# Kernel optimization log

Measured on AMD Instinct MI355X. Metric: run time of the kernel, lower is better.

The kernel has to match this reference:

```python
import jax, jax.numpy as jnp
import numpy as np
from jax import lax

B, C, H0, W0 = 8, 128, 62, 62
G, K, DIL, STRIDE, PAD = 4, 3, 1, 1, 1
P = K * K
GC = C // G
OFFSET_SCALE = 1.0


def setup_inputs() -> dict:
    key = jax.random.key(0)
    ks = jax.random.split(key, 10)
    s = 0.05
    return {
        "x": jax.random.normal(ks[0], (B, C, H0, W0), jnp.float32),
        "conv_w": jax.random.normal(ks[1], (C, C, 1, 1), jnp.float32) * s,
        "conv_b": jax.random.normal(ks[2], (C,), jnp.float32) * s,
        "in_proj_w": jax.random.normal(ks[3], (C, C), jnp.float32) * s,
        "in_proj_b": jnp.zeros((C,), jnp.float32),
        "dw_w": jax.random.normal(ks[4], (C, 1, K, K), jnp.float32) * s,
        "dw_b": jnp.zeros((C,), jnp.float32),
        "ln_g": jnp.ones((C,), jnp.float32),
        "ln_b": jnp.zeros((C,), jnp.float32),
        "off_w": jax.random.normal(ks[5], (C, G * P * 2), jnp.float32) * s,
        "off_b": jax.random.normal(ks[6], (G * P * 2,), jnp.float32) * s,
        "mask_w": jax.random.normal(ks[7], (C, G * P), jnp.float32) * s,
        "mask_b": jnp.zeros((G * P,), jnp.float32),
        "out_proj_w": jax.random.normal(ks[8], (C, C), jnp.float32) * s,
        "out_proj_b": jnp.zeros((C,), jnp.float32),
    }


def _bilinear_sample(img, ix, iy, Hp, Wp):
    # img: [B, G, Hp*Wp, GC] flattened spatial; ix, iy: [B, G, Q, P] pixel coords.
    # Matches torch grid_sample(bilinear, zeros, align_corners=False).
    x0 = jnp.floor(ix)
    y0 = jnp.floor(iy)

    def gather(xi, yi):
        valid = (xi >= 0) & (xi <= Wp - 1) & (yi >= 0) & (yi <= Hp - 1)
        xc = jnp.clip(xi, 0, Wp - 1).astype(jnp.int32)
        yc = jnp.clip(yi, 0, Hp - 1).astype(jnp.int32)
        lin = (yc * Wp + xc).reshape(img.shape[0], img.shape[1], -1)  # [B,G,Q*P]
        v = jnp.take_along_axis(img, lin[..., None], axis=2)          # [B,G,Q*P,GC]
        v = v.reshape(xi.shape + (img.shape[-1],))
        return v * valid[..., None].astype(img.dtype)

    wx1 = (ix - x0)[..., None]
    wx0 = 1.0 - wx1
    wy1 = (iy - y0)[..., None]
    wy0 = 1.0 - wy1
    return (gather(x0, y0) * wx0 * wy0
            + gather(x0 + 1.0, y0) * wx1 * wy0
            + gather(x0, y0 + 1.0) * wx0 * wy1
            + gather(x0 + 1.0, y0 + 1.0) * wx1 * wy1)


def _dcnv3_core(x_proj, offset, mask):
    # x_proj: [B,H,W,C] NHWC; offset: [B,H,W,G*P*2]; mask: [B,H,W,G*P] (softmaxed)
    Bn, H, W, _ = x_proj.shape
    xp = jnp.pad(x_proj, ((0, 0), (PAD, PAD), (PAD, PAD), (0, 0)))
    Hp, Wp = H + 2 * PAD, W + 2 * PAD  # H_out == H for K=3, PAD=1, STRIDE=1
    # reference points (normalized to padded size)
    ref_x = (jnp.arange(W, dtype=jnp.float32) * STRIDE + (DIL * (K - 1)) / 2.0 + 0.5) / Wp
    ref_y = (jnp.arange(H, dtype=jnp.float32) * STRIDE + (DIL * (K - 1)) / 2.0 + 0.5) / Hp
    ref = jnp.stack(jnp.broadcast_arrays(ref_x[None, :], ref_y[:, None]), -1)  # [H,W,2] (x,y)
    # dilation grid (same ordering as torch.meshgrid(x_lin, y_lin))
    klin = (jnp.arange(K, dtype=jnp.float32) * DIL - (DIL * (K - 1)) // 2)
    gx, gy = jnp.meshgrid(klin, klin, indexing='ij')
    grid = jnp.stack([gx / Wp, gy / Hp], -1).reshape(P, 2)
    grid = jnp.tile(grid[None], (G, 1, 1)).reshape(G * P, 2)
    spatial_norm = jnp.array([Wp, Hp], jnp.float32)
    loc = (ref[:, :, None, :] + grid[None, None] * OFFSET_SCALE)[None] \
        + offset.reshape(Bn, H, W, G * P, 2) * OFFSET_SCALE / spatial_norm
    g = 2.0 * loc - 1.0  # normalized grid in [-1,1]
    ix = ((g[..., 0] + 1.0) * Wp - 1.0) / 2.0  # align_corners=False unnormalize
    iy = ((g[..., 1] + 1.0) * Hp - 1.0) / 2.0
    Q = H * W
    ix = ix.reshape(Bn, Q, G, P).transpose(0, 2, 1, 3)  # [B,G,Q,P]
    iy = iy.reshape(Bn, Q, G, P).transpose(0, 2, 1, 3)
    img = xp.reshape(Bn, Hp * Wp, G, GC).transpose(0, 2, 1, 3)  # [B,G,S,GC]
    sampled = _bilinear_sample(img, ix, iy, Hp, Wp)             # [B,G,Q,P,GC]
    m = mask.reshape(Bn, Q, G, P).transpose(0, 2, 1, 3)
    out = jnp.einsum('bgqpc,bgqp->bqgc', sampled, m)
    return out.reshape(Bn, H, W, G * GC)


def reference(x, conv_w, conv_b, in_proj_w, in_proj_b, dw_w, dw_b, ln_g, ln_b,
              off_w, off_b, mask_w, mask_b, out_proj_w, out_proj_b):
    dn = ('NCHW', 'OIHW', 'NCHW')
    # 1x1 conv with padding=1 (spatial grows by 2 on each dim)
    y = lax.conv_general_dilated(x, conv_w, (1, 1), ((PAD, PAD), (PAD, PAD)),
                                 dimension_numbers=dn) + conv_b[None, :, None, None]
    t = y.transpose(0, 2, 3, 1)  # NHWC
    x_proj = t @ in_proj_w + in_proj_b
    # offset/mask branch: depthwise conv + LayerNorm + GELU
    d = lax.conv_general_dilated(y, dw_w, (1, 1), ((1, 1), (1, 1)),
                                 dimension_numbers=dn,
                                 feature_group_count=C) + dw_b[None, :, None, None]
    d = d.transpose(0, 2, 3, 1)
    mu = d.mean(-1, keepdims=True)
    var = ((d - mu) ** 2).mean(-1, keepdims=True)
    d = (d - mu) / jnp.sqrt(var + 1e-5) * ln_g + ln_b
    d = jax.nn.gelu(d, approximate=False)
    offset = d @ off_w + off_b
    Bn, H, W, _ = d.shape
    m = jax.nn.softmax((d @ mask_w + mask_b).reshape(Bn, H, W, G, P), axis=-1)
    out = _dcnv3_core(x_proj, offset, m.reshape(Bn, H, W, G * P))
    out = out @ out_proj_w + out_proj_b
    return out.transpose(0, 3, 1, 2)  # back to NCHW
```

## Files before the change

### kernel.cpp

```cpp
#include <hip/hip_runtime.h>
#include <math.h>

#define BB 8
#define CH 128
#define HH 64
#define WWID 64
#define HIN 62
#define WIN 62
#define SPIN (HIN*WIN)
#define HP 66
#define WP 66
#define GG 4
#define GCH 32
#define NPIX (BB*HH*WWID)
#define ASTRIDE 136

typedef _Float16 v8h __attribute__((ext_vector_type(8)));
typedef _Float16 v4h __attribute__((ext_vector_type(4)));
typedef float    v4f __attribute__((ext_vector_type(4)));

__global__ __launch_bounds__(256) void p0_pack(const float* __restrict__ conv_w,
                                               const float* __restrict__ in_proj_w,
                                               const float* __restrict__ off_w,
                                               const float* __restrict__ mask_w,
                                               const float* __restrict__ out_proj_w,
                                               const float* __restrict__ dw_w,
                                               _Float16* __restrict__ wp,
                                               float* __restrict__ dwT) {
    int t = threadIdx.x;
    if (blockIdx.x == 31) {
        if (t < 128) {
            #pragma unroll
            for (int tap = 0; tap < 9; tap++) dwT[tap * 128 + t] = dw_w[t * 9 + tap];
        }
        return;
    }
    int tid = blockIdx.x * 256 + t;
    int mat, base;
    if (tid < 2048)      { mat = 0; base = 0; }
    else if (tid < 4096) { mat = 1; base = 2048; }
    else if (tid < 5888) { mat = 2; base = 4096; }
    else                 { mat = 3; base = 5888; }
    int fi = tid - base;
    int nt = fi >> 8, rem = fi & 255, kc = rem >> 6, lane = rem & 63;
    int n = nt * 16 + (lane & 15);
    int kbase = kc * 32 + ((lane >> 4) & 3) * 8;
    _Float16* dst = wp + (size_t)tid * 8;
    #pragma unroll
    for (int j = 0; j < 8; j++) {
        int k = kbase + j;
        float v;
        if (mat == 0)      v = conv_w[n * CH + k];
        else if (mat == 1) v = in_proj_w[k * CH + n];
        else if (mat == 2) v = (n < 72) ? off_w[k * 72 + n]
                               : (n < 108 ? mask_w[k * 36 + (n - 72)] : 0.f);
        else               v = out_proj_w[k * CH + n];
        dst[j] = (_Float16)v;
    }
}

__device__ inline void mfma_loop8(const _Float16* __restrict__ a16,
                                  const _Float16* __restrict__ wp,
                                  v4f acc[4], int t) {
    int lane = t & 63;
    int wv = t >> 6;
    int mt = wv >> 1, ntb = (wv & 1) * 4;
    const _Float16* abase = a16 + (mt * 16 + (lane & 15)) * ASTRIDE + ((lane >> 4) * 8);
    #pragma unroll
    for (int kc = 0; kc < 4; kc++) {
        v8h av = *(const v8h*)(abase + kc * 32);
        #pragma unroll
        for (int j = 0; j < 4; j++) {
            v8h bv = *(const v8h*)(wp + ((size_t)((ntb + j) * 4 + kc) * 64 + lane) * 8);
            acc[j] = __builtin_amdgcn_mfma_f32_16x16x32_f16(av, bv, acc[j], 0, 0, 0);
        }
    }
}

__device__ inline void acc_to_a16_8(_Float16* a16, v4f acc[4], int t) {
    int lane = t & 63, ncol = lane & 15;
    int wv = t >> 6;
    int m0 = (wv >> 1) * 16 + ((lane >> 4) * 4);
    int ntb = (wv & 1) * 4;
    #pragma unroll
    for (int j = 0; j < 4; j++)
        #pragma unroll
        for (int r = 0; r < 4; r++)
            a16[(m0 + r) * ASTRIDE + (ntb + j) * 16 + ncol] = (_Float16)acc[j][r];
}

__global__ __launch_bounds__(512) void gA_conv_inproj(const float* __restrict__ x,
                                                      const _Float16* __restrict__ wp_conv,
                                                      const _Float16* __restrict__ wp_in,
                                                      const float* __restrict__ conv_b,
                                                      const float* __restrict__ in_b,
                                                      _Float16* __restrict__ y16,
                                                      _Float16* __restrict__ xpad16) {
    __shared__ _Float16 a16[64 * ASTRIDE];
    int pix0 = blockIdx.x * 64;
    int t = threadIdx.x;
    int h = (pix0 >> 6) & 63, b = pix0 >> 12;
    bool hin = (h >= 1 && h <= 62);
    for (int q = t; q < 8192; q += 512) {
        int c = q >> 6, w = q & 63;
        float v = 0.f;
        if (hin && w >= 1 && w <= 62)
            v = x[((size_t)(b * CH + c)) * SPIN + (h - 1) * WIN + (w - 1)];
        a16[w * ASTRIDE + c] = (_Float16)v;
    }
    __syncthreads();
    int lane = t & 63, ncol = lane & 15;
    int ntb = ((t >> 6) & 1) * 4;
    v4f acc[4];
    #pragma unroll
    for (int j = 0; j < 4; j++) {
        float bv = conv_b[(ntb + j) * 16 + ncol];
        acc[j] = (v4f){bv, bv, bv, bv};
    }
    mfma_loop8(a16, wp_conv, acc, t);
    __syncthreads();
    acc_to_a16_8(a16, acc, t);
    __syncthreads();
    {
        _Float16* dst = y16 + (size_t)pix0 * CH;
        for (int q = t; q < 1024; q += 512)
            *(v8h*)&dst[q * 8] = *(const v8h*)&a16[(q >> 4) * ASTRIDE + (q & 15) * 8];
    }
    v4f acc2[4];
    #pragma unroll
    for (int j = 0; j < 4; j++) {
        float bv = in_b[(ntb + j) * 16 + ncol];
        acc2[j] = (v4f){bv, bv, bv, bv};
    }
    mfma_loop8(a16, wp_in, acc2, t);
    __syncthreads();
    acc_to_a16_8(a16, acc2, t);
    __syncthreads();
    {
        _Float16* dst = xpad16 + (size_t)(((b * HP) + h + 1) * WP + 1) * CH;
        for (int q = t; q < 1024; q += 512)
            *(v8h*)&dst[q * 8] = *(const v8h*)&a16[(q >> 4) * ASTRIDE + (q & 15) * 8];
    }
}

__global__ __launch_bounds__(512) void gF_dwln_offmask(const _Float16* __restrict__ y16,
                                                       const _Float16* __restrict__ wp_om,
                                                       const float* __restrict__ dwT,
                                                       const float* __restrict__ dw_b,
                                                       const float* __restrict__ ln_g,
                                                       const float* __restrict__ ln_b,
                                                       const float* __restrict__ off_b,
                                                       const float* __restrict__ mask_b,
                                                       float* __restrict__ tapmeta) {
    __shared__ char smem[49920];
    _Float16* ylds = (_Float16*)smem;
    int t = threadIdx.x;
    int pix0 = blockIdx.x * 64;
    int h = (pix0 >> 6) & 63, b = pix0 >> 12;
    if (h == 0 || h == 63) {
        for (int i = t; i < 3120; i += 512) *(v8h*)&ylds[i * 8] = (v8h)(_Float16)0;
        __syncthreads();
    }
    for (int idx = t; idx < 3072; idx += 512) {
        int r = idx >> 10, w = (idx >> 4) & 63, c8 = idx & 15;
        int hh = h + r - 1;
        if (hh >= 0 && hh <= 63) {
            v8h v = *(const v8h*)&y16[(size_t)(((b * 64 + hh) * 64 + w) * CH) + c8 * 8];
            *(v8h*)&ylds[(size_t)((r * 16 + c8) * 65 + w) * 8] = v;
        }
    }
    __syncthreads();
    int px = t >> 3, q8 = t & 7;
    float acc[16];
    #pragma unroll
    for (int cb = 0; cb < 4; cb++) *(float4*)&acc[cb * 4] = *(const float4*)&dw_b[q8 * 16 + cb * 4];
    #pragma unroll
    for (int r = 0; r < 3; r++) {
        #pragma unroll
        for (int kx = 0; kx < 3; kx++) {
            int wq = px + kx - 1;
            bool valid = (wq >= 0 && wq <= 63);
            int wpc = min(max(wq, 0), 63);
            int tap = r * 3 + kx;
            if (valid) {
                #pragma unroll
                for (int cb = 0; cb < 2; cb++) {
                    v8h yv = *(const v8h*)&ylds[(size_t)((r * 16 + q8 * 2 + cb) * 65 + wpc) * 8];
                    float4 wa = *(const float4*)&dwT[tap * 128 + q8 * 16 + cb * 8];
                    float4 wb = *(const float4*)&dwT[tap * 128 + q8 * 16 + cb * 8 + 4];
                    acc[cb*8+0] += (float)yv[0] * wa.x; acc[cb*8+1] += (float)yv[1] * wa.y;
                    acc[cb*8+2] += (float)yv[2] * wa.z; acc[cb*8+3] += (float)yv[3] * wa.w;
                    acc[cb*8+4] += (float)yv[4] * wb.x; acc[cb*8+5] += (float)yv[5] * wb.y;
                    acc[cb*8+6] += (float)yv[6] * wb.z; acc[cb*8+7] += (float)yv[7] * wb.w;
                }
            }
        }
    }
    float s = 0.f, ss = 0.f;
    #pragma unroll
    for (int j = 0; j < 16; j++) { s += acc[j]; ss += acc[j] * acc[j]; }
    s  += __shfl_xor(s, 1);  s  += __shfl_xor(s, 2);  s  += __shfl_xor(s, 4);
    ss += __shfl_xor(ss, 1); ss += __shfl_xor(ss, 2); ss += __shfl_xor(ss, 4);
    float mu = s * (1.f / 128.f);
    float var = ss * (1.f / 128.f) - mu * mu;
    float rstd = rsqrtf(var + 1e-5f);
    v8h dreg[2];
    #pragma unroll
    for (int cb = 0; cb < 2; cb++) {
        float4 ga = *(const float4*)&ln_g[q8 * 16 + cb * 8];
        float4 gb = *(const float4*)&ln_g[q8 * 16 + cb * 8 + 4];
        float4 ba = *(const float4*)&ln_b[q8 * 16 + cb * 8];
        float4 bb = *(const float4*)&ln_b[q8 * 16 + cb * 8 + 4];
        float gv[8] = {ga.x, ga.y, ga.z, ga.w, gb.x, gb.y, gb.z, gb.w};
        float bv[8] = {ba.x, ba.y, ba.z, ba.w, bb.x, bb.y, bb.z, bb.w};
        #pragma unroll
        for (int j = 0; j < 8; j++) {
            float xln = (acc[cb * 8 + j] - mu) * rstd * gv[j] + bv[j];
            float gel = 0.5f * xln * (1.f + erff(xln * 0.70710678118654752f));
            dreg[cb][j] = (_Float16)gel;
        }
    }
    __syncthreads();
    _Float16* a16 = (_Float16*)smem;
    float* om = (float*)(smem + 17408);
    #pragma unroll
    for (int cb = 0; cb < 2; cb++)
        *(v8h*)&a16[px * ASTRIDE + q8 * 16 + cb * 8] = dreg[cb];
    __syncthreads();
    int lane = t & 63, ncol = lane & 15;
    int ntb = ((t >> 6) & 1) * 4;
    v4f macc[4];
    #pragma unroll
    for (int j = 0; j < 4; j++) {
        int n = (ntb + j) * 16 + ncol;
        float bv = (n < 72) ? off_b[n] : (n < 108 ? mask_b[n - 72] : 0.f);
        macc[j] = (v4f){bv, bv, bv, bv};
    }
    mfma_loop8(a16, wp_om, macc, t);
    int m0 = ((t >> 6) >> 1) * 16 + ((lane >> 4) * 4);
    #pragma unroll
    for (int j = 0; j < 4; j++) {
        if (ntb + j < 7) {
            #pragma unroll
            for (int r = 0; r < 4; r++)
                om[(m0 + r) * 112 + (ntb + j) * 16 + ncol] = macc[j][r];
        }
    }
    __syncthreads();
    if (t < 256) {
        int pxs = t >> 2, gx = t & 3;
        const float* row = &om[pxs * 112];
        float lg[9];
        #pragma unroll
        for (int i = 0; i < 9; i++) lg[i] = row[72 + gx * 9 + i];
        float mx = lg[0];
        #pragma unroll
        for (int i = 1; i < 9; i++) mx = fmaxf(mx, lg[i]);
        float e[9], sum = 0.f;
        #pragma unroll
        for (int i = 0; i < 9; i++) { e[i] = expf(lg[i] - mx); sum += e[i]; }
        float inv = 1.f / sum;
        float* tm = tapmeta + ((size_t)(pix0 + pxs) * 36 + gx * 9) * 8;
        #pragma unroll
        for (int p = 0; p < 9; p++) {
            int gp = gx * 9 + p;
            float offx = row[gp * 2];
            float offy = row[gp * 2 + 1];
            float m = e[p] * inv;
            float ix = (float)(pxs + (p / 3)) + offx;
            float iy = (float)(h + (p % 3)) + offy;
            float x0f = floorf(ix), y0f = floorf(iy);
            float fx = ix - x0f, fy = iy - y0f;
            int x0 = (int)x0f, y0 = (int)y0f;
            int xi[4] = { x0, x0 + 1, x0,     x0 + 1 };
            int yi[4] = { y0, y0,     y0 + 1, y0 + 1 };
            float wt[4] = { m * (1.f - fx) * (1.f - fy), m * fx * (1.f - fy),
                            m * (1.f - fx) * fy,         m * fx * fy };
            int lo[4];
            #pragma unroll
            for (int cnr = 0; cnr < 4; cnr++) {
                bool vv = ((unsigned)xi[cnr] < (unsigned)WP) && ((unsigned)yi[cnr] < (unsigned)HP);
                int xc = min(max(xi[cnr], 0), WP - 1), yc = min(max(yi[cnr], 0), HP - 1);
                lo[cnr] = (yc * WP + xc) * CH;
                if (!vv) wt[cnr] = 0.f;
            }
            *(int4*)&tm[p * 8]       = make_int4(lo[0], lo[1], lo[2], lo[3]);
            *(float4*)&tm[p * 8 + 4] = make_float4(wt[0], wt[1], wt[2], wt[3]);
        }
    }
}

__global__ __launch_bounds__(256) void kD_gather(const _Float16* __restrict__ xpad16,
                                                 const float* __restrict__ tapmeta,
                                                 _Float16* __restrict__ core16) {
    __shared__ float meta[8 * 36 * 8];
    int t = threadIdx.x;
    int pix0 = blockIdx.x * 8;
    const float4* src = (const float4*)(tapmeta + (size_t)pix0 * 36 * 8);
    for (int i = t; i < 576; i += 256) ((float4*)meta)[i] = src[i];
    __syncthreads();
    int px_l = t >> 5, lane5 = t & 31;
    int c4 = lane5 * 4, g = lane5 >> 3;
    int pix = pix0 + px_l;
    int b = pix >> 12;
    const _Float16* base = xpad16 + (size_t)b * HP * WP * CH + c4;
    float a0 = 0.f, a1 = 0.f, a2 = 0.f, a3 = 0.f;
    #pragma unroll
    for (int p = 0; p < 9; p++) {
        const float* rec = &meta[(size_t)(px_l * 36 + g * 9 + p) * 8];
        int4   o  = *(const int4*)rec;
        float4 wv = *(const float4*)(rec + 4);
        v4h h0 = *(const v4h*)&base[o.x];
        v4h h1 = *(const v4h*)&base[o.y];
        v4h h2 = *(const v4h*)&base[o.z];
        v4h h3 = *(const v4h*)&base[o.w];
        a0 += wv.x*(float)h0[0] + wv.y*(float)h1[0] + wv.z*(float)h2[0] + wv.w*(float)h3[0];
        a1 += wv.x*(float)h0[1] + wv.y*(float)h1[1] + wv.z*(float)h2[1] + wv.w*(float)h3[1];
        a2 += wv.x*(float)h0[2] + wv.y*(float)h1[2] + wv.z*(float)h2[2] + wv.w*(float)h3[2];
        a3 += wv.x*(float)h0[3] + wv.y*(float)h1[3] + wv.z*(float)h2[3] + wv.w*(float)h3[3];
    }
    v4h res = { (_Float16)a0, (_Float16)a1, (_Float16)a2, (_Float16)a3 };
    *(v4h*)&core16[(size_t)pix * CH + c4] = res;
}

__global__ __launch_bounds__(512) void g4_outproj(const _Float16* __restrict__ core16,
                                                  const _Float16* __restrict__ wp,
                                                  const float* __restrict__ bias,
                                                  float* __restrict__ out) {
    __shared__ _Float16 a16[64 * ASTRIDE];
    __shared__ float res[64 * 129];
    int pix0 = blockIdx.x * 64;
    int t = threadIdx.x;
    const _Float16* src = core16 + (size_t)pix0 * CH;
    for (int q = t; q < 1024; q += 512)
        *(v8h*)&a16[(q >> 4) * ASTRIDE + (q & 15) * 8] = *(const v8h*)&src[q * 8];
    __syncthreads();
    int lane = t & 63, ncol = lane & 15;
    int ntb = ((t >> 6) & 1) * 4;
    v4f acc[4];
    #pragma unroll
    for (int j = 0; j < 4; j++) {
        float bv = bias[(ntb + j) * 16 + ncol];
        acc[j] = (v4f){bv, bv, bv, bv};
    }
    mfma_loop8(a16, wp, acc, t);
    int m0 = ((t >> 6) >> 1) * 16 + ((lane >> 4) * 4);
    #pragma unroll
    for (int j = 0; j < 4; j++)
        #pragma unroll
        for (int r = 0; r < 4; r++)
            res[(m0 + r) * 129 + (ntb + j) * 16 + ncol] = acc[j][r];
    __syncthreads();
    int b = pix0 >> 12, h = (pix0 >> 6) & 63;
    for (int q = t; q < 8192; q += 512) {
        int cc = q >> 6, ww = q & 63;
        out[(size_t)((b * CH + cc) * HH + h) * WWID + ww] = res[ww * 129 + cc];
    }
}

extern "C" void kernel_launch(void* const* d_in, const int* in_sizes, int n_in,
                              void* d_out, int out_size, void* d_ws, size_t ws_size,
                              hipStream_t stream) {
    const float* x        = (const float*)d_in[0];
    const float* conv_w   = (const float*)d_in[1];
    const float* conv_b   = (const float*)d_in[2];
    const float* in_proj_w= (const float*)d_in[3];
    const float* in_proj_b= (const float*)d_in[4];
    const float* dw_w     = (const float*)d_in[5];
    const float* dw_b     = (const float*)d_in[6];
    const float* ln_g     = (const float*)d_in[7];
    const float* ln_b     = (const float*)d_in[8];
    const float* off_w    = (const float*)d_in[9];
    const float* off_b    = (const float*)d_in[10];
    const float* mask_w   = (const float*)d_in[11];
    const float* mask_b   = (const float*)d_in[12];
    const float* out_proj_w = (const float*)d_in[13];
    const float* out_proj_b = (const float*)d_in[14];
    float* out = (float*)d_out;

    float* ws = (float*)d_ws;
    const size_t O_WP   = 0;
    const size_t O_DWT  = 32768;
    const size_t O_Y16  = 34816;
    const size_t O_XP16 = O_Y16 + 2097152;
    const size_t O_C16  = O_XP16 + 2230272;
    const size_t O_TM   = O_C16 + 2097152;
    _Float16* wp     = (_Float16*)(ws + O_WP);
    float*    dwT    = ws + O_DWT;
    _Float16* y16    = (_Float16*)(ws + O_Y16);
    _Float16* xpad16 = (_Float16*)(ws + O_XP16);
    _Float16* core16 = (_Float16*)(ws + O_C16);
    float*    tapmeta= ws + O_TM;

    _Float16* wp_conv = wp;
    _Float16* wp_in   = wp + (size_t)2048 * 8;
    _Float16* wp_om   = wp + (size_t)4096 * 8;
    _Float16* wp_out  = wp + (size_t)5888 * 8;

    p0_pack<<<32, 256, 0, stream>>>(conv_w, in_proj_w, off_w, mask_w, out_proj_w, dw_w, wp, dwT);
    hipMemsetAsync(xpad16, 0, (size_t)8 * HP * WP * CH * sizeof(_Float16), stream);
    gA_conv_inproj<<<NPIX / 64, 512, 0, stream>>>(x, wp_conv, wp_in, conv_b, in_proj_b, y16, xpad16);
    gF_dwln_offmask<<<NPIX / 64, 512, 0, stream>>>(y16, wp_om, dwT, dw_b, ln_g, ln_b, off_b, mask_b, tapmeta);
    kD_gather<<<NPIX / 8, 256, 0, stream>>>(xpad16, tapmeta, core16);
    g4_outproj<<<NPIX / 64, 512, 0, stream>>>(core16, wp_out, out_proj_b, out);
}
```

Baseline: 173.8 us.

## Fuse deformable gather into output projection and vectorize global loads/stores

Merges the bilinear gather kernel with the output-projection GEMM so the sampled core values go straight into shared memory instead of through a global fp16 buffer. Each thread now gathers 16 channels with 8-wide half loads per corner. The input conv staging and the NCHW output write are also vectorized to float4 accesses. In exchange, the fused kernel uses more shared memory and registers per block, which may lower occupancy and latency hiding for the gather.

```diff
diff --git a/kernel.cpp b/kernel.cpp
--- a/kernel.cpp
+++ b/kernel.cpp
@@ -18,6 +18,7 @@
 typedef _Float16 v8h __attribute__((ext_vector_type(8)));
 typedef _Float16 v4h __attribute__((ext_vector_type(4)));
 typedef float    v4f __attribute__((ext_vector_type(4)));
+typedef float    f4a __attribute__((ext_vector_type(4), aligned(4)));
 
 __global__ __launch_bounds__(256) void p0_pack(const float* __restrict__ conv_w,
                                                const float* __restrict__ in_proj_w,
@@ -101,12 +102,19 @@
     int t = threadIdx.x;
     int h = (pix0 >> 6) & 63, b = pix0 >> 12;
     bool hin = (h >= 1 && h <= 62);
-    for (int q = t; q < 8192; q += 512) {
-        int c = q >> 6, w = q & 63;
-        float v = 0.f;
-        if (hin && w >= 1 && w <= 62)
-            v = x[((size_t)(b * CH + c)) * SPIN + (h - 1) * WIN + (w - 1)];
-        a16[w * ASTRIDE + c] = (_Float16)v;
+    for (int q = t; q < 2048; q += 512) {
+        int c = q >> 4, w4 = (q & 15) * 4;
+        float4 v = make_float4(0.f, 0.f, 0.f, 0.f);
+        if (hin) {
+            const float* xr = x + ((size_t)(b * CH + c)) * SPIN + (h - 1) * WIN;
+            if (w4 == 0)       { f4a e = *(const f4a*)&xr[0];      v = make_float4(0.f, e[0], e[1], e[2]); }
+            else if (w4 == 60) { f4a e = *(const f4a*)&xr[58];     v = make_float4(e[1], e[2], e[3], 0.f); }
+            else               { f4a e = *(const f4a*)&xr[w4 - 1]; v = make_float4(e[0], e[1], e[2], e[3]); }
+        }
+        a16[(w4 + 0) * ASTRIDE + c] = (_Float16)v.x;
+        a16[(w4 + 1) * ASTRIDE + c] = (_Float16)v.y;
+        a16[(w4 + 2) * ASTRIDE + c] = (_Float16)v.z;
+        a16[(w4 + 3) * ASTRIDE + c] = (_Float16)v.w;
     }
     __syncthreads();
     int lane = t & 63, ncol = lane & 15;
@@ -290,71 +298,73 @@
     }
 }
 
-__global__ __launch_bounds__(256) void kD_gather(const _Float16* __restrict__ xpad16,
-                                                 const float* __restrict__ tapmeta,
-                                                 _Float16* __restrict__ core16) {
-    __shared__ float meta[8 * 36 * 8];
+__global__ __launch_bounds__(512) void g5_gather_outproj(const _Float16* __restrict__ xpad16,
+                                                         const float* __restrict__ tapmeta,
+                                                         const _Float16* __restrict__ wp,
+                                                         const float* __restrict__ bias,
+                                                         float* __restrict__ out) {
+    __shared__ char smem[50432];
+    _Float16* a16 = (_Float16*)smem;
+    float* res = (float*)(smem + 17408);
     int t = threadIdx.x;
-    int pix0 = blockIdx.x * 8;
-    const float4* src = (const float4*)(tapmeta + (size_t)pix0 * 36 * 8);
-    for (int i = t; i < 576; i += 256) ((float4*)meta)[i] = src[i];
-    __syncthreads();
-    int px_l = t >> 5, lane5 = t & 31;
-    int c4 = lane5 * 4, g = lane5 >> 3;
-    int pix = pix0 + px_l;
-    int b = pix >> 12;
-    const _Float16* base = xpad16 + (size_t)b * HP * WP * CH + c4;
-    float a0 = 0.f, a1 = 0.f, a2 = 0.f, a3 = 0.f;
+    int pix0 = blockIdx.x * 64;
+    int b = pix0 >> 12, h = (pix0 >> 6) & 63;
+    int px = t >> 3, s = t & 7;
+    int ch = s * 16, g = s >> 1;
+    int pix = pix0 + px;
+    const _Float16* base = xpad16 + (size_t)b * HP * WP * CH + ch;
+    const float* tmbase = tapmeta + ((size_t)pix * 36 + g * 9) * 8;
+    float acc[16];
+    #pragma unroll
+    for (int j = 0; j < 16; j++) acc[j] = 0.f;
     #pragma unroll
     for (int p = 0; p < 9; p++) {
-        const float* rec = &meta[(size_t)(px_l * 36 + g * 9 + p) * 8];
-        int4   o  = *(const int4*)rec;
-        float4 wv = *(const float4*)(rec + 4);
-        v4h h0 = *(const v4h*)&base[o.x];
-        v4h h1 = *(const v4h*)&base[o.y];
-        v4h h2 = *(const v4h*)&base[o.z];
-        v4h h3 = *(const v4h*)&base[o.w];
-        a0 += wv.x*(float)h0[0] + wv.y*(float)h1[0] + wv.z*(float)h2[0] + wv.w*(float)h3[0];
-        a1 += wv.x*(float)h0[1] + wv.y*(float)h1[1] + wv.z*(float)h2[1] + wv.w*(float)h3[1];
-        a2 += wv.x*(float)h0[2] + wv.y*(float)h1[2] + wv.z*(float)h2[2] + wv.w*(float)h3[2];
-        a3 += wv.x*(float)h0[3] + wv.y*(float)h1[3] + wv.z*(float)h2[3] + wv.w*(float)h3[3];
-    }
-    v4h res = { (_Float16)a0, (_Float16)a1, (_Float16)a2, (_Float16)a3 };
-    *(v4h*)&core16[(size_t)pix * CH + c4] = res;
-}
-
-__global__ __launch_bounds__(512) void g4_outproj(const _Float16* __restrict__ core16,
-                                                  const _Float16* __restrict__ wp,
-                                                  const float* __restrict__ bias,
-                                                  float* __restrict__ out) {
-    __shared__ _Float16 a16[64 * ASTRIDE];
-    __shared__ float res[64 * 129];
-    int pix0 = blockIdx.x * 64;
-    int t = threadIdx.x;
-    const _Float16* src = core16 + (size_t)pix0 * CH;
-    for (int q = t; q < 1024; q += 512)
-        *(v8h*)&a16[(q >> 4) * ASTRIDE + (q & 15) * 8] = *(const v8h*)&src[q * 8];
+        int4   o  = *(const int4*)&tmbase[p * 8];
+        float4 wv = *(const float4*)&tmbase[p * 8 + 4];
+        v8h c0a = *(const v8h*)&base[o.x];
+        v8h c0b = *(const v8h*)&base[o.x + 8];
+        v8h c1a = *(const v8h*)&base[o.y];
+        v8h c1b = *(const v8h*)&base[o.y + 8];
+        v8h c2a = *(const v8h*)&base[o.z];
+        v8h c2b = *(const v8h*)&base[o.z + 8];
+        v8h c3a = *(const v8h*)&base[o.w];
+        v8h c3b = *(const v8h*)&base[o.w + 8];
+        #pragma unroll
+        for (int j = 0; j < 8; j++) {
+            acc[j]     += wv.x*(float)c0a[j] + wv.y*(float)c1a[j] + wv.z*(float)c2a[j] + wv.w*(float)c3a[j];
+            acc[j + 8] += wv.x*(float)c0b[j] + wv.y*(float)c1b[j] + wv.z*(float)c2b[j] + wv.w*(float)c3b[j];
+        }
+    }
+    v8h r0, r1;
+    #pragma unroll
+    for (int j = 0; j < 8; j++) { r0[j] = (_Float16)acc[j]; r1[j] = (_Float16)acc[j + 8]; }
+    *(v8h*)&a16[px * ASTRIDE + ch]     = r0;
+    *(v8h*)&a16[px * ASTRIDE + ch + 8] = r1;
     __syncthreads();
     int lane = t & 63, ncol = lane & 15;
     int ntb = ((t >> 6) & 1) * 4;
-    v4f acc[4];
+    v4f macc[4];
     #pragma unroll
     for (int j = 0; j < 4; j++) {
         float bv = bias[(ntb + j) * 16 + ncol];
-        acc[j] = (v4f){bv, bv, bv, bv};
-    }
-    mfma_loop8(a16, wp, acc, t);
+        macc[j] = (v4f){bv, bv, bv, bv};
+    }
+    mfma_loop8(a16, wp, macc, t);
     int m0 = ((t >> 6) >> 1) * 16 + ((lane >> 4) * 4);
     #pragma unroll
     for (int j = 0; j < 4; j++)
         #pragma unroll
         for (int r = 0; r < 4; r++)
-            res[(m0 + r) * 129 + (ntb + j) * 16 + ncol] = acc[j][r];
-    __syncthreads();
-    int b = pix0 >> 12, h = (pix0 >> 6) & 63;
-    for (int q = t; q < 8192; q += 512) {
-        int cc = q >> 6, ww = q & 63;
-        out[(size_t)((b * CH + cc) * HH + h) * WWID + ww] = res[ww * 129 + cc];
+            res[(m0 + r) * 129 + (ntb + j) * 16 + ncol] = macc[j][r];
+    __syncthreads();
+    for (int q = t; q < 2048; q += 512) {
+        int cc = q >> 4, w4 = (q & 15) * 4;
+        float4 o;
+        o.x = res[(w4 + 0) * 129 + cc];
+        o.y = res[(w4 + 1) * 129 + cc];
+        o.z = res[(w4 + 2) * 129 + cc];
+        o.w = res[(w4 + 3) * 129 + cc];
+        *(float4*)&out[(size_t)((b * CH + cc) * HH + h) * WWID + w4] = o;
     }
 }
 
@@ -383,13 +393,11 @@
     const size_t O_DWT  = 32768;
     const size_t O_Y16  = 34816;
     const size_t O_XP16 = O_Y16 + 2097152;
-    const size_t O_C16  = O_XP16 + 2230272;
-    const size_t O_TM   = O_C16 + 2097152;
+    const size_t O_TM   = O_XP16 + 2230272;
     _Float16* wp     = (_Float16*)(ws + O_WP);
     float*    dwT    = ws + O_DWT;
     _Float16* y16    = (_Float16*)(ws + O_Y16);
     _Float16* xpad16 = (_Float16*)(ws + O_XP16);
-    _Float16* core16 = (_Float16*)(ws + O_C16);
     float*    tapmeta= ws + O_TM;
 
     _Float16* wp_conv = wp;
@@ -401,6 +409,5 @@
     hipMemsetAsync(xpad16, 0, (size_t)8 * HP * WP * CH * sizeof(_Float16), stream);
     gA_conv_inproj<<<NPIX / 64, 512, 0, stream>>>(x, wp_conv, wp_in, conv_b, in_proj_b, y16, xpad16);
     gF_dwln_offmask<<<NPIX / 64, 512, 0, stream>>>(y16, wp_om, dwT, dw_b, ln_g, ln_b, off_b, mask_b, tapmeta);
-    kD_gather<<<NPIX / 8, 256, 0, stream>>>(xpad16, tapmeta, core16);
-    g4_outproj<<<NPIX / 64, 512, 0, stream>>>(core16, wp_out, out_proj_b, out);
-}
+    g5_gather_outproj<<<NPIX / 64, 512, 0, stream>>>(xpad16, tapmeta, wp_out, out_proj_b, out);
+}
```

Measured after the change: 239.5 us. 37.8% more time.

## Pad gather source with extra zero border, compress tap metadata, vectorize I/O

Applied to the files above, without the earlier changes.

The padded x_proj buffer grows to 70x70 with a two-pixel zero guard ring, so bilinear corners never need per-corner validity checks or clamping. Sample coordinates are clamped into the guard range instead. Tap metadata shrinks from 8 to 4 floats per tap (one base offset plus fx, fy, mask), and the four corner weights are rebuilt inside the gather kernel, halving metadata traffic. The NCHW input load and output store switch to float4 accesses, which costs strided LDS scatter and gather in exchange for a somewhat larger memset.

```diff
diff --git a/kernel.cpp b/kernel.cpp
--- a/kernel.cpp
+++ b/kernel.cpp
@@ -10,6 +10,7 @@
 #define SPIN (HIN*WIN)
 #define HP 66
 #define WP 66
+#define GP2 70
 #define GG 4
 #define GCH 32
 #define NPIX (BB*HH*WWID)
@@ -18,6 +19,7 @@
 typedef _Float16 v8h __attribute__((ext_vector_type(8)));
 typedef _Float16 v4h __attribute__((ext_vector_type(4)));
 typedef float    v4f __attribute__((ext_vector_type(4)));
+typedef float    f4a __attribute__((ext_vector_type(4), aligned(4)));
 
 __global__ __launch_bounds__(256) void p0_pack(const float* __restrict__ conv_w,
                                                const float* __restrict__ in_proj_w,
@@ -101,12 +103,19 @@
     int t = threadIdx.x;
     int h = (pix0 >> 6) & 63, b = pix0 >> 12;
     bool hin = (h >= 1 && h <= 62);
-    for (int q = t; q < 8192; q += 512) {
-        int c = q >> 6, w = q & 63;
-        float v = 0.f;
-        if (hin && w >= 1 && w <= 62)
-            v = x[((size_t)(b * CH + c)) * SPIN + (h - 1) * WIN + (w - 1)];
-        a16[w * ASTRIDE + c] = (_Float16)v;
+    for (int q = t; q < 2048; q += 512) {
+        int c = q >> 4, w4 = (q & 15) * 4;
+        float4 v = make_float4(0.f, 0.f, 0.f, 0.f);
+        if (hin) {
+            const float* xr = x + ((size_t)(b * CH + c)) * SPIN + (h - 1) * WIN;
+            if (w4 == 0)       { f4a e = *(const f4a*)&xr[0];      v = make_float4(0.f, e[0], e[1], e[2]); }
+            else if (w4 == 60) { f4a e = *(const f4a*)&xr[58];     v = make_float4(e[1], e[2], e[3], 0.f); }
+            else               { f4a e = *(const f4a*)&xr[w4 - 1]; v = make_float4(e[0], e[1], e[2], e[3]); }
+        }
+        a16[(w4 + 0) * ASTRIDE + c] = (_Float16)v.x;
+        a16[(w4 + 1) * ASTRIDE + c] = (_Float16)v.y;
+        a16[(w4 + 2) * ASTRIDE + c] = (_Float16)v.z;
+        a16[(w4 + 3) * ASTRIDE + c] = (_Float16)v.w;
     }
     __syncthreads();
     int lane = t & 63, ncol = lane & 15;
@@ -137,7 +146,7 @@
     acc_to_a16_8(a16, acc2, t);
     __syncthreads();
     {
-        _Float16* dst = xpad16 + (size_t)(((b * HP) + h + 1) * WP + 1) * CH;
+        _Float16* dst = xpad16 + (size_t)(((b * GP2) + h + 3) * GP2 + 3) * CH;
         for (int q = t; q < 1024; q += 512)
             *(v8h*)&dst[q * 8] = *(const v8h*)&a16[(q >> 4) * ASTRIDE + (q & 15) * 8];
     }
@@ -260,7 +269,7 @@
         #pragma unroll
         for (int i = 0; i < 9; i++) { e[i] = expf(lg[i] - mx); sum += e[i]; }
         float inv = 1.f / sum;
-        float* tm = tapmeta + ((size_t)(pix0 + pxs) * 36 + gx * 9) * 8;
+        float* tm = tapmeta + ((size_t)(pix0 + pxs) * 36 + gx * 9) * 4;
         #pragma unroll
         for (int p = 0; p < 9; p++) {
             int gp = gx * 9 + p;
@@ -269,23 +278,16 @@
             float m = e[p] * inv;
             float ix = (float)(pxs + (p / 3)) + offx;
             float iy = (float)(h + (p % 3)) + offy;
+            ix = fminf(fmaxf(ix, -2.f), (float)(WP + 1));
+            iy = fminf(fmaxf(iy, -2.f), (float)(HP + 1));
             float x0f = floorf(ix), y0f = floorf(iy);
             float fx = ix - x0f, fy = iy - y0f;
             int x0 = (int)x0f, y0 = (int)y0f;
-            int xi[4] = { x0, x0 + 1, x0,     x0 + 1 };
-            int yi[4] = { y0, y0,     y0 + 1, y0 + 1 };
-            float wt[4] = { m * (1.f - fx) * (1.f - fy), m * fx * (1.f - fy),
-                            m * (1.f - fx) * fy,         m * fx * fy };
-            int lo[4];
-            #pragma unroll
-            for (int cnr = 0; cnr < 4; cnr++) {
-                bool vv = ((unsigned)xi[cnr] < (unsigned)WP) && ((unsigned)yi[cnr] < (unsigned)HP);
-                int xc = min(max(xi[cnr], 0), WP - 1), yc = min(max(yi[cnr], 0), HP - 1);
-                lo[cnr] = (yc * WP + xc) * CH;
-                if (!vv) wt[cnr] = 0.f;
-            }
-            *(int4*)&tm[p * 8]       = make_int4(lo[0], lo[1], lo[2], lo[3]);
-            *(float4*)&tm[p * 8 + 4] = make_float4(wt[0], wt[1], wt[2], wt[3]);
+            int off = ((y0 + 2) * GP2 + (x0 + 2)) * CH;
+            float4 rec;
+            rec.x = __int_as_float(off);
+            rec.y = fx; rec.z = fy; rec.w = m;
+            *(float4*)&tm[p * 4] = rec;
         }
     }
 }
@@ -293,31 +295,36 @@
 __global__ __launch_bounds__(256) void kD_gather(const _Float16* __restrict__ xpad16,
                                                  const float* __restrict__ tapmeta,
                                                  _Float16* __restrict__ core16) {
-    __shared__ float meta[8 * 36 * 8];
+    __shared__ float meta[8 * 36 * 4];
     int t = threadIdx.x;
     int pix0 = blockIdx.x * 8;
-    const float4* src = (const float4*)(tapmeta + (size_t)pix0 * 36 * 8);
-    for (int i = t; i < 576; i += 256) ((float4*)meta)[i] = src[i];
+    const float4* src = (const float4*)(tapmeta + (size_t)pix0 * 36 * 4);
+    for (int i = t; i < 288; i += 256) ((float4*)meta)[i] = src[i];
     __syncthreads();
     int px_l = t >> 5, lane5 = t & 31;
     int c4 = lane5 * 4, g = lane5 >> 3;
     int pix = pix0 + px_l;
     int b = pix >> 12;
-    const _Float16* base = xpad16 + (size_t)b * HP * WP * CH + c4;
+    const _Float16* base = xpad16 + (size_t)b * GP2 * GP2 * CH + c4;
     float a0 = 0.f, a1 = 0.f, a2 = 0.f, a3 = 0.f;
     #pragma unroll
     for (int p = 0; p < 9; p++) {
-        const float* rec = &meta[(size_t)(px_l * 36 + g * 9 + p) * 8];
-        int4   o  = *(const int4*)rec;
-        float4 wv = *(const float4*)(rec + 4);
-        v4h h0 = *(const v4h*)&base[o.x];
-        v4h h1 = *(const v4h*)&base[o.y];
-        v4h h2 = *(const v4h*)&base[o.z];
-        v4h h3 = *(const v4h*)&base[o.w];
-        a0 += wv.x*(float)h0[0] + wv.y*(float)h1[0] + wv.z*(float)h2[0] + wv.w*(float)h3[0];
-        a1 += wv.x*(float)h0[1] + wv.y*(float)h1[1] + wv.z*(float)h2[1] + wv.w*(float)h3[1];
-        a2 += wv.x*(float)h0[2] + wv.y*(float)h1[2] + wv.z*(float)h2[2] + wv.w*(float)h3[2];
-        a3 += wv.x*(float)h0[3] + wv.y*(float)h1[3] + wv.z*(float)h2[3] + wv.w*(float)h3[3];
+        float4 rec = *(const float4*)&meta[(size_t)(px_l * 36 + g * 9 + p) * 4];
+        int off = __float_as_int(rec.x);
+        float fx = rec.y, fy = rec.z, m = rec.w;
+        float w11 = fx * fy;
+        float w10 = fx - w11;
+        float w01 = fy - w11;
+        float w00 = 1.f - fx - fy + w11;
+        w00 *= m; w10 *= m; w01 *= m; w11 *= m;
+        v4h h0 = *(const v4h*)&base[off];
+        v4h h1 = *(const v4h*)&base[off + CH];
+        v4h h2 = *(const v4h*)&base[off + GP2 * CH];
+        v4h h3 = *(const v4h*)&base[off + GP2 * CH + CH];
+        a0 += w00*(float)h0[0] + w10*(float)h1[0] + w01*(float)h2[0] + w11*(float)h3[0];
+        a1 += w00*(float)h0[1] + w10*(float)h1[1] + w01*(float)h2[1] + w11*(float)h3[1];
+        a2 += w00*(float)h0[2] + w10*(float)h1[2] + w01*(float)h2[2] + w11*(float)h3[2];
+        a3 += w00*(float)h0[3] + w10*(float)h1[3] + w01*(float)h2[3] + w11*(float)h3[3];
     }
     v4h res = { (_Float16)a0, (_Float16)a1, (_Float16)a2, (_Float16)a3 };
     *(v4h*)&core16[(size_t)pix * CH + c4] = res;
@@ -352,9 +359,14 @@
             res[(m0 + r) * 129 + (ntb + j) * 16 + ncol] = acc[j][r];
     __syncthreads();
     int b = pix0 >> 12, h = (pix0 >> 6) & 63;
-    for (int q = t; q < 8192; q += 512) {
-        int cc = q >> 6, ww = q & 63;
-        out[(size_t)((b * CH + cc) * HH + h) * WWID + ww] = res[ww * 129 + cc];
+    for (int q = t; q < 2048; q += 512) {
+        int cc = q >> 4, w4 = (q & 15) * 4;
+        float4 o;
+        o.x = res[(w4 + 0) * 129 + cc];
+        o.y = res[(w4 + 1) * 129 + cc];
+        o.z = res[(w4 + 2) * 129 + cc];
+        o.w = res[(w4 + 3) * 129 + cc];
+        *(float4*)&out[(size_t)((b * CH + cc) * HH + h) * WWID + w4] = o;
     }
 }
 
@@ -383,7 +395,7 @@
     const size_t O_DWT  = 32768;
     const size_t O_Y16  = 34816;
     const size_t O_XP16 = O_Y16 + 2097152;
-    const size_t O_C16  = O_XP16 + 2230272;
+    const size_t O_C16  = O_XP16 + 2508800;
     const size_t O_TM   = O_C16 + 2097152;
     _Float16* wp     = (_Float16*)(ws + O_WP);
     float*    dwT    = ws + O_DWT;
@@ -398,7 +410,7 @@
     _Float16* wp_out  = wp + (size_t)5888 * 8;
 
     p0_pack<<<32, 256, 0, stream>>>(conv_w, in_proj_w, off_w, mask_w, out_proj_w, dw_w, wp, dwT);
-    hipMemsetAsync(xpad16, 0, (size_t)8 * HP * WP * CH * sizeof(_Float16), stream);
+    hipMemsetAsync(xpad16, 0, (size_t)8 * GP2 * GP2 * CH * sizeof(_Float16), stream);
     gA_conv_inproj<<<NPIX / 64, 512, 0, stream>>>(x, wp_conv, wp_in, conv_b, in_proj_b, y16, xpad16);
     gF_dwln_offmask<<<NPIX / 64, 512, 0, stream>>>(y16, wp_om, dwT, dw_b, ln_g, ln_b, off_b, mask_b, tapmeta);
     kD_gather<<<NPIX / 8, 256, 0, stream>>>(xpad16, tapmeta, core16);
```

New measurement: 165.6 us. -4.7%, faster.
